# Kernel tuning notes

Measured on AMD Instinct MI355X. Metric: run time of the kernel, lower is better.

Reference implementation:

```python
import jax, jax.numpy as jnp
import numpy as np

NUM_HEADS = 32
NUM_KV_HEADS = 8
HEAD_DIM = 128
ROPE_THETA = 10000.0
NEG_INF = -1e9


def _rope_cos_sin(position_ids, head_dim, dtype):
    # inv_freq: [head_dim/2]
    inv_freq = 1.0 / (ROPE_THETA ** (jnp.arange(0, head_dim, 2, dtype=jnp.float32) / head_dim))
    # freqs: [B, S, head_dim/2]
    freqs = position_ids.astype(jnp.float32)[..., None] * inv_freq[None, None, :]
    emb = jnp.concatenate([freqs, freqs], axis=-1)  # [B, S, head_dim]
    return jnp.cos(emb).astype(dtype), jnp.sin(emb).astype(dtype)


def _rotate_half(x):
    x1, x2 = jnp.split(x, 2, axis=-1)
    return jnp.concatenate([-x2, x1], axis=-1)


def setup_inputs() -> dict:
    key = jax.random.key(0)
    k1, k2, k3, k4, k5 = jax.random.split(key, 5)
    B, S, H = 2, 2048, 4096
    scale = 1.0 / np.sqrt(H)
    return {
        "hidden_states": jax.random.normal(k1, (B, S, H), jnp.float32),
        "position_ids": jnp.broadcast_to(jnp.arange(S, dtype=jnp.int32)[None, :], (B, S)),
        "Wq": jax.random.normal(k2, (H, H), jnp.float32) * scale,
        "Wk": jax.random.normal(k3, (NUM_KV_HEADS * HEAD_DIM, H), jnp.float32) * scale,
        "Wv": jax.random.normal(k4, (NUM_KV_HEADS * HEAD_DIM, H), jnp.float32) * scale,
        "Wo": jax.random.normal(k5, (H, H), jnp.float32) * scale,
    }


def reference(hidden_states, position_ids, Wq, Wk, Wv, Wo):
    B, S, H = hidden_states.shape
    dtype = hidden_states.dtype
    n_rep = NUM_HEADS // NUM_KV_HEADS

    # QKV projections (torch Linear: x @ W.T)
    q = (hidden_states @ Wq.T).reshape(B, S, NUM_HEADS, HEAD_DIM).transpose(0, 2, 1, 3)
    k = (hidden_states @ Wk.T).reshape(B, S, NUM_KV_HEADS, HEAD_DIM).transpose(0, 2, 1, 3)
    v = (hidden_states @ Wv.T).reshape(B, S, NUM_KV_HEADS, HEAD_DIM).transpose(0, 2, 1, 3)

    # RoPE (cos/sin broadcast over heads)
    cos, sin = _rope_cos_sin(position_ids, HEAD_DIM, dtype)
    cos, sin = cos[:, None, :, :], sin[:, None, :, :]  # [B,1,S,D]
    q = q * cos + _rotate_half(q) * sin
    k = k * cos + _rotate_half(k) * sin

    # repeat_kv (GQA): [B, KVH, S, D] -> [B, KVH*n_rep, S, D]
    k = jnp.repeat(k, n_rep, axis=1)
    v = jnp.repeat(v, n_rep, axis=1)

    # scaled dot-product attention with causal mask, softmax in fp32
    scores = jnp.einsum('bhqd,bhkd->bhqk', q, k) / np.sqrt(HEAD_DIM)
    causal = jnp.tril(jnp.ones((S, S), dtype=bool))
    scores = jnp.where(causal[None, None, :, :], scores, NEG_INF)
    probs = jax.nn.softmax(scores.astype(jnp.float32), axis=-1).astype(dtype)

    attn = jnp.einsum('bhqk,bhkd->bhqd', probs, v)
    attn = attn.transpose(0, 2, 1, 3).reshape(B, S, H)
    return attn @ Wo.T
```

## Files before the change

### kernel.cpp

```cpp
#include <hip/hip_runtime.h>

#define S_LEN 2048
#define BATCH 2
#define HID 4096
#define NH 32
#define NKV 8
#define DH 128
#define MROWS (BATCH*S_LEN)
#define QKV_N 6144

typedef unsigned short u16;
typedef unsigned int u32;
typedef __bf16 bf16x8 __attribute__((ext_vector_type(8)));
typedef float f32x4 __attribute__((ext_vector_type(4)));
typedef u16 u16x8 __attribute__((ext_vector_type(8)));

__device__ __forceinline__ u16 f2bf(float f) {
  union { float f; u32 u; } v; v.f = f;
  return (u16)((v.u + 0x8000u) >> 16);
}
__device__ __forceinline__ float bf2f(u16 h) {
  union { u32 u; float f; } v; v.u = ((u32)h) << 16;
  return v.f;
}
__device__ __forceinline__ u32 cvtpk(float a, float b) {
  u32 r;
  asm("v_cvt_pk_bf16_f32 %0, %1, %2" : "=v"(r) : "v"(a), "v"(b));
  return r;
}
__device__ __forceinline__ void async16(const void* g, void* l) {
  __builtin_amdgcn_global_load_lds(
      (const __attribute__((address_space(1))) u32*)g,
      (__attribute__((address_space(3))) u32*)l, 16, 0, 0);
}
__device__ __forceinline__ f32x4 mfma16(bf16x8 a, bf16x8 b, f32x4 c) {
  return __builtin_amdgcn_mfma_f32_16x16x32_bf16(a, b, c, 0, 0, 0);
}

__global__ __launch_bounds__(256) void cvt_f32_bf16(const float* __restrict__ in,
                                                    u16* __restrict__ out, int n) {
  int i0 = (blockIdx.x * 256 + threadIdx.x) * 8;
  if (i0 >= n) return;
  float4 a = *(const float4*)(in + i0);
  float4 b = *(const float4*)(in + i0 + 4);
  u16x8 r;
  r[0]=f2bf(a.x); r[1]=f2bf(a.y); r[2]=f2bf(a.z); r[3]=f2bf(a.w);
  r[4]=f2bf(b.x); r[5]=f2bf(b.y); r[6]=f2bf(b.z); r[7]=f2bf(b.w);
  *(u16x8*)(out + i0) = r;
}

template<int OUT_BF16>
__global__ __launch_bounds__(512, 2) void gemm256(
    const u16* __restrict__ A, const u16* __restrict__ B, void* __restrict__ Cout,
    int M, int N, int K, int XC, int SR, int SC) {
  __shared__ u16 As[2][2][64 * 128];
  __shared__ u16 Bs[2][2][64 * 128];
  const int NKT = K >> 6;
  int bid = (int)blockIdx.x;
  int xcd = bid & 7, l = bid >> 3;
  int tm = (xcd / XC) * SR + l / SC;
  int tn = (xcd % XC) * SC + l % SC;
  int m0 = tm << 8, n0 = tn << 8;
  int t = threadIdx.x;
  int w = t >> 6, lane = t & 63, lo = lane & 15, hi = lane >> 4;
  int wm = w >> 2, wn = w & 3;
  int rbb = (wn & 1) << 6;

  int srow = (w << 3) + (lane >> 3);
  int scol = (lane & 7) << 3;

  auto stageA = [&](int kt, int buf, int h) {
#pragma unroll
    for (int c2 = 0; c2 < 2; ++c2) {
      int row = (c2 << 6) + srow;
      int col = scol ^ ((row & 7) << 3);
      async16(A + (size_t)(m0 + (h << 7) + row) * K + (kt << 6) + col,
              (char*)&As[buf][h][0] + (c2 << 13) + (w << 10));
    }
  };
  auto stageB = [&](int kt, int buf, int h) {
#pragma unroll
    for (int c2 = 0; c2 < 2; ++c2) {
      int row = (c2 << 6) + srow;
      int col = scol ^ ((row & 7) << 3);
      async16(B + (size_t)(n0 + (h << 7) + row) * K + (kt << 6) + col,
              (char*)&Bs[buf][h][0] + (c2 << 13) + (w << 10));
    }
  };

  const f32x4 fz = {0.f, 0.f, 0.f, 0.f};
  f32x4 acc[8][4];
#pragma unroll
  for (int i = 0; i < 8; ++i)
#pragma unroll
    for (int j = 0; j < 4; ++j) acc[i][j] = fz;
  bf16x8 af[4][2], bf0[2][2], bf1[2][2];

  auto rdA = [&](int c, int half, bf16x8 (&dst)[4][2]) {
    const u16* Ab = &As[c][wm][0];
#pragma unroll
    for (int mf = 0; mf < 4; ++mf)
#pragma unroll
      for (int ks = 0; ks < 2; ++ks) {
        int ra = (half << 6) + (mf << 4) + lo;
        dst[mf][ks] = *(const bf16x8*)(Ab + (ra << 6) +
                      (((ks << 5) + (hi << 3)) ^ ((ra & 7) << 3)));
      }
  };
  auto rdB = [&](int c, int bfrag, bf16x8 (&dst)[2][2]) {
    const u16* Bb = &Bs[c][wn >> 1][0];
#pragma unroll
    for (int nf = 0; nf < 2; ++nf)
#pragma unroll
      for (int ks = 0; ks < 2; ++ks) {
        int rb = rbb + (bfrag << 5) + (nf << 4) + lo;
        dst[nf][ks] = *(const bf16x8*)(Bb + (rb << 6) +
                      (((ks << 5) + (hi << 3)) ^ ((rb & 7) << 3)));
      }
  };
  auto MM = [&](bf16x8 (&a)[4][2], bf16x8 (&b)[2][2], int mo, int no) {
#pragma unroll
    for (int mf = 0; mf < 4; ++mf)
#pragma unroll
      for (int nf = 0; nf < 2; ++nf)
#pragma unroll
        for (int ks = 0; ks < 2; ++ks)
          acc[mo + mf][no + nf] = mfma16(a[mf][ks], b[nf][ks], acc[mo + mf][no + nf]);
  };

#define BAR()    __builtin_amdgcn_s_barrier()
#define LGKM0()  asm volatile("s_waitcnt lgkmcnt(0)" ::: "memory")
#define VM4()    asm volatile("s_waitcnt vmcnt(4)" ::: "memory")
#define PRIO(x)  __builtin_amdgcn_s_setprio(x)

  stageA(0, 0, 0); stageA(0, 0, 1);
  stageB(0, 0, 0); stageB(0, 0, 1);
  stageB(1, 1, 0); stageB(1, 1, 1);
  VM4();
  BAR();

  const int NT = NKT >> 1;
  for (int it = 0; it < NT; ++it) {
    int e = it << 1, o = e + 1;
    int e2 = (e + 2 >= NKT) ? 0 : e + 2;
    int o2 = (o + 2 >= NKT) ? 1 : o + 2;

    rdA(0, 0, af); rdB(0, 0, bf0);
    stageA(o, 1, 0);
    BAR(); LGKM0(); PRIO(1);
    MM(af, bf0, 0, 0);
    PRIO(0); BAR();

    rdB(0, 1, bf1);
    stageA(o, 1, 1);
    BAR(); LGKM0(); PRIO(1);
    MM(af, bf1, 0, 2);
    PRIO(0); BAR();

    rdA(0, 1, af);
    stageB(e2, 0, 0);
    BAR(); LGKM0(); PRIO(1);
    MM(af, bf1, 4, 2);
    PRIO(0); BAR();

    stageB(e2, 0, 1);
    BAR(); PRIO(1);
    MM(af, bf0, 4, 0);
    PRIO(0); VM4(); BAR();

    rdA(1, 0, af); rdB(1, 0, bf0);
    stageA(e2, 0, 0);
    BAR(); LGKM0(); PRIO(1);
    MM(af, bf0, 0, 0);
    PRIO(0); BAR();

    rdB(1, 1, bf1);
    stageA(e2, 0, 1);
    BAR(); LGKM0(); PRIO(1);
    MM(af, bf1, 0, 2);
    PRIO(0); BAR();

    rdA(1, 1, af);
    stageB(o2, 1, 0);
    BAR(); LGKM0(); PRIO(1);
    MM(af, bf1, 4, 2);
    PRIO(0); BAR();

    stageB(o2, 1, 1);
    BAR(); PRIO(1);
    MM(af, bf0, 4, 0);
    PRIO(0); VM4(); BAR();
  }

#undef BAR
#undef LGKM0
#undef VM4
#undef PRIO

#pragma unroll
  for (int mf = 0; mf < 8; ++mf)
#pragma unroll
    for (int nf = 0; nf < 4; ++nf)
#pragma unroll
      for (int r = 0; r < 4; ++r) {
        int row = m0 + (wm << 7) + (mf << 4) + (hi << 2) + r;
        int col = n0 + (wn << 6) + (nf << 4) + lo;
        if (OUT_BF16) ((u16*)Cout)[(size_t)row * N + col] = f2bf(acc[mf][nf][r]);
        else          ((float*)Cout)[(size_t)row * N + col] = acc[mf][nf][r];
      }
}

__global__ __launch_bounds__(256) void rope_kernel(u16* __restrict__ X,
                                                   const int* __restrict__ pos,
                                                   int ncols, int pitch, float scale) {
  int idx = blockIdx.x * 256 + threadIdx.x;
  int groups = ncols >> 3;
  int m = idx / groups;
  int gi = idx - m * groups;
  if (m >= MROWS) return;
  int head = gi >> 4;
  int d0 = (gi & 15) << 2;
  float p = (float)pos[m];
  u16* base = X + (size_t)m * pitch + head * 128;
  u16 xa[4], xb[4], oa[4], ob[4];
  *(uint2*)xa = *(const uint2*)(base + d0);
  *(uint2*)xb = *(const uint2*)(base + d0 + 64);
#pragma unroll
  for (int i = 0; i < 4; ++i) {
    float j = (float)(d0 + i);
    float inv = __expf(j * -0.14391156516030342f);
    float fr = p * inv;
    float s, c;
    sincosf(fr, &s, &c);
    float x1 = bf2f(xa[i]), x2 = bf2f(xb[i]);
    oa[i] = f2bf((x1 * c - x2 * s) * scale);
    ob[i] = f2bf((x2 * c + x1 * s) * scale);
  }
  *(uint2*)(base + d0) = *(uint2*)oa;
  *(uint2*)(base + d0 + 64) = *(uint2*)ob;
}

__global__ __launch_bounds__(256) void transpose_v(const u16* __restrict__ V,
                                                   u16* __restrict__ Vt) {
  int bid = blockIdx.x;
  int s0 = (bid & 31) << 6;
  int bg = bid >> 5;
  int b = bg >> 3, g = bg & 7;
  __shared__ u16 tile[64][128];
  int t = threadIdx.x;
#pragma unroll
  for (int r = 0; r < 4; ++r) {
    int c = (r << 8) + t;
    int row = c >> 4, cc = c & 15;
    *(uint4*)&tile[row][cc * 8] =
        *(const uint4*)(V + (size_t)(b * S_LEN + s0 + row) * QKV_N + g * 128 + cc * 8);
  }
  __syncthreads();
#pragma unroll
  for (int r = 0; r < 4; ++r) {
    int c = (r << 8) + t;
    int d = c >> 3, cs = c & 7;
    u16 tmp[8];
#pragma unroll
    for (int i = 0; i < 8; ++i) tmp[i] = tile[cs * 8 + i][d];
    *(uint4*)(Vt + ((size_t)bg * 128 + d) * S_LEN + s0 + cs * 8) = *(uint4*)tmp;
  }
}

__global__ __launch_bounds__(256) void attn_kernel(
    const u16* __restrict__ Q, const u16* __restrict__ K,
    const u16* __restrict__ Vt, u16* __restrict__ O) {
  int bid = blockIdx.x;
  int qt = 31 - (bid >> 6);
  int bh = bid & 63;
  int b = bh >> 5, h = bh & 31;
  int g = h >> 2;
  __shared__ u16 Kl[64 * 128];
  __shared__ u16 Vl[128 * 64];
  __shared__ u16 Pl[4][16 * 72];
  int t = threadIdx.x, w = t >> 6, lane = t & 63, lo = lane & 15, hi = lane >> 4;

  bf16x8 qf[4];
  {
    const u16* qb = Q + (size_t)(b * S_LEN + (qt << 6) + (w << 4) + lo) * QKV_N + h * 128;
#pragma unroll
    for (int kk = 0; kk < 4; ++kk) qf[kk] = *(const bf16x8*)(qb + kk * 32 + hi * 8);
  }
  const f32x4 fz = {0.f, 0.f, 0.f, 0.f};
  f32x4 acc[8];
#pragma unroll
  for (int f = 0; f < 8; ++f) acc[f] = fz;
  float mrun = -1e30f, lrun = 0.f;

  const u16* Kbase = K + (size_t)(b * S_LEN) * QKV_N + g * 128;
  const u16* Vbase = Vt + (size_t)((b << 3) + g) * 128 * S_LEN;

  int ntiles = qt + 1;
  for (int tile = 0; tile < ntiles; ++tile) {
    int s0 = tile << 6;
#pragma unroll
    for (int r = 0; r < 4; ++r) {
      int c = (r << 8) + (w << 6) + lane;
      int row = c >> 4, cc = c & 15;
      int src = cc ^ (row & 7);
      async16(Kbase + (size_t)(s0 + row) * QKV_N + src * 8,
              (char*)Kl + (r << 12) + (w << 10));
    }
#pragma unroll
    for (int r = 0; r < 4; ++r) {
      int c = (r << 8) + (w << 6) + lane;
      int row = c >> 3, cc = c & 7;
      int src = cc ^ (row & 7);
      async16(Vbase + (size_t)row * S_LEN + s0 + src * 8,
              (char*)Vl + (r << 12) + (w << 10));
    }
    __syncthreads();

    f32x4 sf[4];
#pragma unroll
    for (int j = 0; j < 4; ++j) {
      f32x4 sv = fz;
#pragma unroll
      for (int kk = 0; kk < 4; ++kk) {
        int row = (j << 4) + lo;
        int ch = ((kk << 2) + hi) ^ (row & 7);
        bf16x8 kf = *(const bf16x8*)(Kl + row * 128 + ch * 8);
        sv = __builtin_amdgcn_mfma_f32_16x16x32_bf16(kf, qf[kk], sv, 0, 0, 0);
      }
      sf[j] = sv;
    }
    if (tile == qt) {
      int q_rel = (w << 4) + lo;
#pragma unroll
      for (int j = 0; j < 4; ++j)
#pragma unroll
        for (int r = 0; r < 4; ++r)
          if (((j << 4) + (hi << 2) + r) > q_rel) sf[j][r] = -1e9f;
    }
    float pmax = sf[0][0];
#pragma unroll
    for (int j = 0; j < 4; ++j)
#pragma unroll
      for (int r = 0; r < 4; ++r) pmax = fmaxf(pmax, sf[j][r]);
    pmax = fmaxf(pmax, __shfl_xor(pmax, 16, 64));
    pmax = fmaxf(pmax, __shfl_xor(pmax, 32, 64));
    if (__any(pmax > mrun + 8.f)) {
      float mn = fmaxf(mrun, pmax);
      float fsc = __expf(mrun - mn);
      mrun = mn;
      lrun *= fsc;
#pragma unroll
      for (int f = 0; f < 8; ++f)
#pragma unroll
        for (int r = 0; r < 4; ++r) acc[f][r] *= fsc;
    }
    float psum = 0.f;
#pragma unroll
    for (int j = 0; j < 4; ++j)
#pragma unroll
      for (int r = 0; r < 4; ++r) {
        float p = __expf(sf[j][r] - mrun);
        sf[j][r] = p;
        psum += p;
      }
    psum += __shfl_xor(psum, 16, 64);
    psum += __shfl_xor(psum, 32, 64);
    lrun += psum;

#pragma unroll
    for (int j = 0; j < 4; ++j) {
      uint2 pk;
      pk.x = cvtpk(sf[j][0], sf[j][1]);
      pk.y = cvtpk(sf[j][2], sf[j][3]);
      *(uint2*)&Pl[w][lo * 72 + (j << 4) + (hi << 2)] = pk;
    }
#pragma unroll
    for (int kk = 0; kk < 2; ++kk) {
      bf16x8 pf = *(const bf16x8*)&Pl[w][lo * 72 + (kk << 5) + (hi << 3)];
#pragma unroll
      for (int f = 0; f < 8; ++f) {
        int vrow = (f << 4) + lo;
        int phys = ((kk << 2) + hi) ^ (vrow & 7);
        bf16x8 vf = *(const bf16x8*)(Vl + vrow * 64 + phys * 8);
        acc[f] = __builtin_amdgcn_mfma_f32_16x16x32_bf16(vf, pf, acc[f], 0, 0, 0);
      }
    }
    __syncthreads();
  }

  float rl = 1.0f / lrun;
#pragma unroll
  for (int half = 0; half < 2; ++half) {
#pragma unroll
    for (int f2 = 0; f2 < 4; ++f2) {
      int f = (half << 2) + f2;
      uint2 pk;
      pk.x = cvtpk(acc[f][0] * rl, acc[f][1] * rl);
      pk.y = cvtpk(acc[f][2] * rl, acc[f][3] * rl);
      *(uint2*)&Pl[w][lo * 72 + (f2 << 4) + (hi << 2)] = pk;
    }
#pragma unroll
    for (int it = 0; it < 2; ++it) {
      int rowq = (lane >> 3) + (it << 3);
      int c8 = lane & 7;
      uint4 val = *(const uint4*)&Pl[w][rowq * 72 + c8 * 8];
      *(uint4*)(O + (size_t)(b * S_LEN + (qt << 6) + (w << 4) + rowq) * 4096 +
                h * 128 + (half << 6) + c8 * 8) = val;
    }
  }
}

extern "C" void kernel_launch(void* const* d_in, const int* in_sizes, int n_in,
                              void* d_out, int out_size, void* d_ws, size_t ws_size,
                              hipStream_t stream) {
  const float* hidden = (const float*)d_in[0];
  const int* pos = (const int*)d_in[1];
  const float* Wq = (const float*)d_in[2];
  const float* Wk = (const float*)d_in[3];
  const float* Wv = (const float*)d_in[4];
  const float* Wo = (const float*)d_in[5];
  float* out = (float*)d_out;

  u16* hb   = (u16*)d_ws;
  u16* wqb  = hb   + 16777216;
  u16* wkb  = wqb  + 16777216;
  u16* wvb  = wkb  + 4194304;
  u16* wob  = wvb  + 4194304;
  u16* QKVb = wob  + 16777216;
  u16* Vtb  = QKVb + 25165824;
  u16* Ob   = Vtb  + 4194304;

  cvt_f32_bf16<<<8192, 256, 0, stream>>>(hidden, hb, 16777216);
  cvt_f32_bf16<<<8192, 256, 0, stream>>>(Wq, wqb, 16777216);
  cvt_f32_bf16<<<2048, 256, 0, stream>>>(Wk, wkb, 4194304);
  cvt_f32_bf16<<<2048, 256, 0, stream>>>(Wv, wvb, 4194304);
  cvt_f32_bf16<<<8192, 256, 0, stream>>>(Wo, wob, 16777216);

  gemm256<1><<<384, 512, 0, stream>>>(hb, wqb, QKVb, 4096, QKV_N, 4096, 4, 8, 6);

  rope_kernel<<<8192, 256, 0, stream>>>(QKVb, pos, 4096, QKV_N, 0.08838834764831845f);
  rope_kernel<<<2048, 256, 0, stream>>>(QKVb + 4096, pos, 1024, QKV_N, 1.0f);

  transpose_v<<<512, 256, 0, stream>>>(QKVb + 5120, Vtb);

  attn_kernel<<<2048, 256, 0, stream>>>(QKVb, QKVb + 4096, Vtb, Ob);

  gemm256<0><<<256, 512, 0, stream>>>(Ob, wob, out, 4096, 4096, 4096, 2, 4, 8);
}
```

Baseline: 539.3 us.

## Add 256x128-tile triple-buffered GEMM for QKV projection

Adds a new GEMM kernel with a 256x128 output tile, a three-stage LDS ring buffer and a single-k-tile pipeline, and uses it for the QKV projection with twice as many workgroups (768 instead of 384). The goal is better load balance across CUs, since 384 large tiles fill the GPU poorly, and more latency hiding from the deeper prefetch. In exchange, each tile reuses A data less, and LDS use per block goes up, which may limit occupancy. The output projection still uses the original 256x256 kernel.

Result: slower. 580.4 us (+7.6%).

```diff
diff --git a/kernel.cpp b/kernel.cpp
--- a/kernel.cpp
+++ b/kernel.cpp
@@ -36,6 +36,10 @@
 __device__ __forceinline__ f32x4 mfma16(bf16x8 a, bf16x8 b, f32x4 c) {
   return __builtin_amdgcn_mfma_f32_16x16x32_bf16(a, b, c, 0, 0, 0);
 }
+
+#define BAR()    __builtin_amdgcn_s_barrier()
+#define LGKM0()  asm volatile("s_waitcnt lgkmcnt(0)" ::: "memory")
+#define PRIO(x)  __builtin_amdgcn_s_setprio(x)
 
 __global__ __launch_bounds__(256) void cvt_f32_bf16(const float* __restrict__ in,
                                                     u16* __restrict__ out, int n) {
@@ -128,11 +132,7 @@
           acc[mo + mf][no + nf] = mfma16(a[mf][ks], b[nf][ks], acc[mo + mf][no + nf]);
   };
 
-#define BAR()    __builtin_amdgcn_s_barrier()
-#define LGKM0()  asm volatile("s_waitcnt lgkmcnt(0)" ::: "memory")
 #define VM4()    asm volatile("s_waitcnt vmcnt(4)" ::: "memory")
-#define PRIO(x)  __builtin_amdgcn_s_setprio(x)
-
   stageA(0, 0, 0); stageA(0, 0, 1);
   stageB(0, 0, 0); stageB(0, 0, 1);
   stageB(1, 1, 0); stageB(1, 1, 1);
@@ -191,11 +191,7 @@
     MM(af, bf0, 4, 0);
     PRIO(0); VM4(); BAR();
   }
-
-#undef BAR
-#undef LGKM0
 #undef VM4
-#undef PRIO
 
 #pragma unroll
   for (int mf = 0; mf < 8; ++mf)
@@ -205,6 +201,126 @@
       for (int r = 0; r < 4; ++r) {
         int row = m0 + (wm << 7) + (mf << 4) + (hi << 2) + r;
         int col = n0 + (wn << 6) + (nf << 4) + lo;
+        if (OUT_BF16) ((u16*)Cout)[(size_t)row * N + col] = f2bf(acc[mf][nf][r]);
+        else          ((float*)Cout)[(size_t)row * N + col] = acc[mf][nf][r];
+      }
+}
+
+template<int OUT_BF16>
+__global__ __launch_bounds__(512, 2) void gemm256n128(
+    const u16* __restrict__ A, const u16* __restrict__ B, void* __restrict__ Cout,
+    int M, int N, int K, int XC, int SR, int SC) {
+  __shared__ u16 As[3][2][64 * 128];
+  __shared__ u16 Bs[3][64 * 128];
+  const int NKT = K >> 6;
+  int bid = (int)blockIdx.x;
+  int xcd = bid & 7, l = bid >> 3;
+  int tm = (xcd / XC) * SR + l / SC;
+  int tn = (xcd % XC) * SC + l % SC;
+  int m0 = tm << 8, n0 = tn << 7;
+  int t = threadIdx.x;
+  int w = t >> 6, lane = t & 63, lo = lane & 15, hi = lane >> 4;
+  int wm = w >> 2, wn = w & 3;
+
+  int srow = (w << 3) + (lane >> 3);
+  int scol = (lane & 7) << 3;
+
+  auto stageA = [&](int kt, int buf) {
+#pragma unroll
+    for (int h = 0; h < 2; ++h)
+#pragma unroll
+      for (int c2 = 0; c2 < 2; ++c2) {
+        int row = (c2 << 6) + srow;
+        int col = scol ^ ((row & 7) << 3);
+        async16(A + (size_t)(m0 + (h << 7) + row) * K + (kt << 6) + col,
+                (char*)&As[buf][h][0] + (c2 << 13) + (w << 10));
+      }
+  };
+  auto stageB = [&](int kt, int buf) {
+#pragma unroll
+    for (int c2 = 0; c2 < 2; ++c2) {
+      int row = (c2 << 6) + srow;
+      int col = scol ^ ((row & 7) << 3);
+      async16(B + (size_t)(n0 + row) * K + (kt << 6) + col,
+              (char*)&Bs[buf][0] + (c2 << 13) + (w << 10));
+    }
+  };
+
+  const f32x4 fz = {0.f, 0.f, 0.f, 0.f};
+  f32x4 acc[8][2];
+#pragma unroll
+  for (int i = 0; i < 8; ++i)
+#pragma unroll
+    for (int j = 0; j < 2; ++j) acc[i][j] = fz;
+  bf16x8 af[4][2], bfv[2][2];
+
+  auto rdA = [&](int c, int half) {
+    const u16* Ab = &As[c][wm][0];
+#pragma unroll
+    for (int mf = 0; mf < 4; ++mf)
+#pragma unroll
+      for (int ks = 0; ks < 2; ++ks) {
+        int ra = (half << 6) + (mf << 4) + lo;
+        af[mf][ks] = *(const bf16x8*)(Ab + (ra << 6) +
+                      (((ks << 5) + (hi << 3)) ^ ((ra & 7) << 3)));
+      }
+  };
+  auto rdB = [&](int c) {
+    const u16* Bb = &Bs[c][0];
+#pragma unroll
+    for (int nf = 0; nf < 2; ++nf)
+#pragma unroll
+      for (int ks = 0; ks < 2; ++ks) {
+        int rb = (wn << 5) + (nf << 4) + lo;
+        bfv[nf][ks] = *(const bf16x8*)(Bb + (rb << 6) +
+                      (((ks << 5) + (hi << 3)) ^ ((rb & 7) << 3)));
+      }
+  };
+  auto MM = [&](int mo) {
+#pragma unroll
+    for (int mf = 0; mf < 4; ++mf)
+#pragma unroll
+      for (int nf = 0; nf < 2; ++nf)
+#pragma unroll
+        for (int ks = 0; ks < 2; ++ks)
+          acc[mo + mf][nf] = mfma16(af[mf][ks], bfv[nf][ks], acc[mo + mf][nf]);
+  };
+
+#define VM6()    asm volatile("s_waitcnt vmcnt(6)" ::: "memory")
+  stageA(0, 0); stageB(0, 0);
+  stageA(1, 1); stageB(1, 1);
+  VM6();
+  BAR();
+
+  int c = 0;
+  for (int kt = 0; kt < NKT; ++kt) {
+    int kn = kt + 2; if (kn >= NKT) kn -= NKT;
+    int cn = c + 2; if (cn >= 3) cn -= 3;
+
+    rdA(c, 0); rdB(c);
+    stageA(kn, cn);
+    BAR(); LGKM0(); PRIO(1);
+    MM(0);
+    PRIO(0); BAR();
+
+    rdA(c, 1);
+    stageB(kn, cn);
+    BAR(); LGKM0(); PRIO(1);
+    MM(4);
+    PRIO(0); VM6(); BAR();
+
+    ++c; if (c >= 3) c = 0;
+  }
+#undef VM6
+
+#pragma unroll
+  for (int mf = 0; mf < 8; ++mf)
+#pragma unroll
+    for (int nf = 0; nf < 2; ++nf)
+#pragma unroll
+      for (int r = 0; r < 4; ++r) {
+        int row = m0 + (wm << 7) + (mf << 4) + (hi << 2) + r;
+        int col = n0 + (wn << 5) + (nf << 4) + lo;
         if (OUT_BF16) ((u16*)Cout)[(size_t)row * N + col] = f2bf(acc[mf][nf][r]);
         else          ((float*)Cout)[(size_t)row * N + col] = acc[mf][nf][r];
       }
@@ -436,7 +552,7 @@
   cvt_f32_bf16<<<2048, 256, 0, stream>>>(Wv, wvb, 4194304);
   cvt_f32_bf16<<<8192, 256, 0, stream>>>(Wo, wob, 16777216);
 
-  gemm256<1><<<384, 512, 0, stream>>>(hb, wqb, QKVb, 4096, QKV_N, 4096, 4, 8, 6);
+  gemm256n128<1><<<768, 512, 0, stream>>>(hb, wqb, QKVb, 4096, QKV_N, 4096, 4, 8, 12);
 
   rope_kernel<<<8192, 256, 0, stream>>>(QKVb, pos, 4096, QKV_N, 0.08838834764831845f);
   rope_kernel<<<2048, 256, 0, stream>>>(QKVb + 4096, pos, 1024, QKV_N, 1.0f);
```

## Replace QKV projection GEMM with 4-wave 256x256 kernel using 4-stage LDS pipeline

Applied to the files above, without the earlier changes.

Adds a new GEMM kernel for the QKV projection that uses 4 waves of 256 threads, each wave computing a 128x128 sub-tile. It streams K in 32-wide slices through a 4-deep LDS ring with async global-to-LDS loads and double-buffered register fragments. The aim is more MFMA work per LDS read and fewer barriers per MFMA than the 8-wave kernel. In exchange it needs a very large accumulator register file (256 floats per lane) and runs at one block per CU, which risks spills and low occupancy.

Result: slower. 669.9 us (+24.2%).

```diff
diff --git a/kernel.cpp b/kernel.cpp
--- a/kernel.cpp
+++ b/kernel.cpp
@@ -36,6 +36,10 @@
 __device__ __forceinline__ f32x4 mfma16(bf16x8 a, bf16x8 b, f32x4 c) {
   return __builtin_amdgcn_mfma_f32_16x16x32_bf16(a, b, c, 0, 0, 0);
 }
+
+#define BAR()    __builtin_amdgcn_s_barrier()
+#define LGKM0()  asm volatile("s_waitcnt lgkmcnt(0)" ::: "memory")
+#define PRIO(x)  __builtin_amdgcn_s_setprio(x)
 
 __global__ __launch_bounds__(256) void cvt_f32_bf16(const float* __restrict__ in,
                                                     u16* __restrict__ out, int n) {
@@ -47,6 +51,123 @@
   r[0]=f2bf(a.x); r[1]=f2bf(a.y); r[2]=f2bf(a.z); r[3]=f2bf(a.w);
   r[4]=f2bf(b.x); r[5]=f2bf(b.y); r[6]=f2bf(b.z); r[7]=f2bf(b.w);
   *(u16x8*)(out + i0) = r;
+}
+
+__global__ __launch_bounds__(256, 1) void gemm4w(
+    const u16* __restrict__ A, const u16* __restrict__ B, u16* __restrict__ Cout,
+    int M, int N, int K, int XC, int SR, int SC) {
+  __shared__ u16 Ab[4][128 * 64];
+  __shared__ u16 Bb[4][128 * 64];
+  const int NKT = K >> 5;
+  int bid = (int)blockIdx.x;
+  int xcd = bid & 7, l = bid >> 3;
+  int tm = (xcd / XC) * SR + l / SC;
+  int tn = (xcd % XC) * SC + l % SC;
+  int m0 = tm << 8, n0 = tn << 8;
+  int t = threadIdx.x;
+  int w = t >> 6, lane = t & 63, lo = lane & 15, hi = lane >> 4;
+  int wm = w >> 1, wn = w & 1;
+
+  int srcrow[4], srckk[4];
+#pragma unroll
+  for (int i = 0; i < 4; ++i) {
+    int id = (i << 8) + t;
+    int R = id >> 3, c = id & 7, sc = c ^ (R & 7);
+    srcrow[i] = (R << 1) + (sc >> 2);
+    srckk[i] = (sc & 3) << 3;
+  }
+  int offA[8], offB[8];
+#pragma unroll
+  for (int f = 0; f < 8; ++f) {
+    int ra = (wm << 7) + (f << 4) + lo;
+    int R = ra >> 1, c = ((((ra & 1) << 2) + hi)) ^ (R & 7);
+    offA[f] = (R << 6) + (c << 3);
+    int rb = (wn << 7) + (f << 4) + lo;
+    int R2 = rb >> 1, c2 = ((((rb & 1) << 2) + hi)) ^ (R2 & 7);
+    offB[f] = (R2 << 6) + (c2 << 3);
+  }
+
+  auto stage = [&](int kt, int buf) {
+    const u16* As = A + (size_t)m0 * K + (kt << 5);
+    const u16* Bs = B + (size_t)n0 * K + (kt << 5);
+#pragma unroll
+    for (int i = 0; i < 4; ++i) {
+      async16(As + (size_t)srcrow[i] * K + srckk[i],
+              (char*)&Ab[buf][0] + (((i << 8) + t) << 4));
+      async16(Bs + (size_t)srcrow[i] * K + srckk[i],
+              (char*)&Bb[buf][0] + (((i << 8) + t) << 4));
+    }
+  };
+
+  f32x4 acc[8][8];
+  const f32x4 fz = {0.f, 0.f, 0.f, 0.f};
+#pragma unroll
+  for (int i = 0; i < 8; ++i)
+#pragma unroll
+    for (int j = 0; j < 8; ++j) acc[i][j] = fz;
+  bf16x8 aX[8], bX[8], aY[8], bY[8];
+
+  auto rd = [&](int buf, bf16x8 (&aT)[8], bf16x8 (&bT)[8]) {
+    const u16* Abase = &Ab[buf][0];
+    const u16* Bbase = &Bb[buf][0];
+#pragma unroll
+    for (int f = 0; f < 8; ++f) {
+      aT[f] = *(const bf16x8*)(Abase + offA[f]);
+      bT[f] = *(const bf16x8*)(Bbase + offB[f]);
+    }
+  };
+  auto MM = [&](bf16x8 (&aT)[8], bf16x8 (&bT)[8]) {
+#pragma unroll
+    for (int mf = 0; mf < 8; ++mf)
+#pragma unroll
+      for (int nf = 0; nf < 8; ++nf)
+        acc[mf][nf] = mfma16(aT[mf], bT[nf], acc[mf][nf]);
+  };
+
+  stage(0, 0); stage(1, 1); stage(2, 2); stage(3, 3);
+  asm volatile("s_waitcnt vmcnt(24)" ::: "memory");
+  BAR();
+  rd(0, aX, bX);
+  LGKM0();
+  BAR();
+
+  const int NJ = NKT >> 1;
+  for (int j = 0; j < NJ; ++j) {
+    int k0 = j << 1, k1 = k0 + 1;
+    {
+      rd((k0 + 1) & 3, aY, bY);
+      PRIO(1);
+      MM(aX, bX);
+      PRIO(0);
+      int ks = k0 + 4; if (ks >= NKT) ks -= NKT;
+      stage(ks, k0 & 3);
+      asm volatile("s_waitcnt vmcnt(16)" ::: "memory");
+      LGKM0();
+      BAR();
+    }
+    {
+      rd((k1 + 1) & 3, aX, bX);
+      PRIO(1);
+      MM(aY, bY);
+      PRIO(0);
+      int ks = k1 + 4; if (ks >= NKT) ks -= NKT;
+      stage(ks, k1 & 3);
+      asm volatile("s_waitcnt vmcnt(16)" ::: "memory");
+      LGKM0();
+      BAR();
+    }
+  }
+
+#pragma unroll
+  for (int mf = 0; mf < 8; ++mf)
+#pragma unroll
+    for (int nf = 0; nf < 8; ++nf)
+#pragma unroll
+      for (int r = 0; r < 4; ++r) {
+        int row = m0 + (wm << 7) + (mf << 4) + (hi << 2) + r;
+        int col = n0 + (wn << 7) + (nf << 4) + lo;
+        Cout[(size_t)row * N + col] = f2bf(acc[mf][nf][r]);
+      }
 }
 
 template<int OUT_BF16>
@@ -128,11 +249,7 @@
           acc[mo + mf][no + nf] = mfma16(a[mf][ks], b[nf][ks], acc[mo + mf][no + nf]);
   };
 
-#define BAR()    __builtin_amdgcn_s_barrier()
-#define LGKM0()  asm volatile("s_waitcnt lgkmcnt(0)" ::: "memory")
 #define VM4()    asm volatile("s_waitcnt vmcnt(4)" ::: "memory")
-#define PRIO(x)  __builtin_amdgcn_s_setprio(x)
-
   stageA(0, 0, 0); stageA(0, 0, 1);
   stageB(0, 0, 0); stageB(0, 0, 1);
   stageB(1, 1, 0); stageB(1, 1, 1);
@@ -191,11 +308,7 @@
     MM(af, bf0, 4, 0);
     PRIO(0); VM4(); BAR();
   }
-
-#undef BAR
-#undef LGKM0
 #undef VM4
-#undef PRIO
 
 #pragma unroll
   for (int mf = 0; mf < 8; ++mf)
@@ -436,7 +549,7 @@
   cvt_f32_bf16<<<2048, 256, 0, stream>>>(Wv, wvb, 4194304);
   cvt_f32_bf16<<<8192, 256, 0, stream>>>(Wo, wob, 16777216);
 
-  gemm256<1><<<384, 512, 0, stream>>>(hb, wqb, QKVb, 4096, QKV_N, 4096, 4, 8, 6);
+  gemm4w<<<384, 256, 0, stream>>>(hb, wqb, QKVb, 4096, QKV_N, 4096, 4, 8, 6);
 
   rope_kernel<<<8192, 256, 0, stream>>>(QKVb, pos, 4096, QKV_N, 0.08838834764831845f);
   rope_kernel<<<2048, 256, 0, stream>>>(QKVb + 4096, pos, 1024, QKV_N, 1.0f);
```
